# Kernel optimization log

Hardware: AMD Instinct MI355X
Metric: run time of the kernel (lower is better)

The kernel has to match this reference:

```python
import jax, jax.numpy as jnp
import numpy as np

N = 20000      # nodes
E = 320000     # edges (avg degree 16)
IN, HID, OUT, H = 128, 32, 32, 8
NEG_SLOPE = 0.2


def _gat_conv(x, src, dst, W, al, ar, b):
    """One DGL-style GATConv. x: [N, F_in], W: [F_in, H*D], al/ar: [H, D], b: [H*D].
    Returns [N, H, D]."""
    n = x.shape[0]
    Hh, D = al.shape
    feat = (x @ W).reshape(n, Hh, D)                      # [N,H,D]
    el = jnp.sum(feat * al[None], axis=-1)                # [N,H]
    er = jnp.sum(feat * ar[None], axis=-1)                # [N,H]
    e = jax.nn.leaky_relu(el[src] + er[dst], NEG_SLOPE)   # [E,H]
    # edge softmax over incoming edges of each dst node (stable)
    emax = jax.ops.segment_max(e, dst, num_segments=n)    # [N,H]
    ee = jnp.exp(e - emax[dst])                           # [E,H]
    denom = jax.ops.segment_sum(ee, dst, num_segments=n)  # [N,H]
    alpha = ee / denom[dst]                               # [E,H]
    msg = feat[src] * alpha[:, :, None]                   # [E,H,D] gather+weight
    out = jax.ops.segment_sum(msg, dst, num_segments=n)   # [N,H,D] scatter-add
    return out + b.reshape(1, Hh, D)


def setup_inputs() -> dict:
    key = jax.random.key(0)
    ks = jax.random.split(key, 11)
    return {
        "x":   jax.random.normal(ks[0], (N, IN), dtype=jnp.float32),
        "src": jax.random.randint(ks[1], (E,), 0, N, dtype=jnp.int32),
        "dst": jax.random.randint(ks[2], (E,), 0, N, dtype=jnp.int32),
        "W1":  jax.random.normal(ks[3], (IN, H * HID), dtype=jnp.float32) * 0.1,
        "al1": jax.random.normal(ks[4], (H, HID), dtype=jnp.float32) * 0.1,
        "ar1": jax.random.normal(ks[5], (H, HID), dtype=jnp.float32) * 0.1,
        "b1":  jnp.zeros((H * HID,), dtype=jnp.float32),
        "W2":  jax.random.normal(ks[6], (HID, H * OUT), dtype=jnp.float32) * 0.1,
        "al2": jax.random.normal(ks[7], (H, OUT), dtype=jnp.float32) * 0.1,
        "ar2": jax.random.normal(ks[8], (H, OUT), dtype=jnp.float32) * 0.1,
        "b2":  jnp.zeros((H * OUT,), dtype=jnp.float32),
    }


def reference(x, src, dst, W1, al1, ar1, b1, W2, al2, ar2, b2):
    h = _gat_conv(x, src, dst, W1, al1, ar1, b1)          # [N,H,HID]
    h = jnp.mean(jax.nn.relu(h), axis=1)                  # [N,HID]
    h = _gat_conv(h, src, dst, W2, al2, ar2, b2)          # [N,H,OUT]
    return jnp.mean(h, axis=1)                            # [N,OUT]
```

## Files before the change

### kernel.cpp

```cpp
#include <hip/hip_runtime.h>
#include <hip/hip_bf16.h>

#define N_NODES 20000
#define N_EDGES 320000
#define F_IN    128
#define F_HID   32
#define NHEAD   8
#define FDIM    256
#define CAP     96

#define GROUPS  313
#define GPAD    16
#define GCAP    2048
#define EPB     2048
#define P1B     ((N_EDGES + EPB - 1) / EPB)

#define TW2     12

typedef __hip_bfloat16 bf16;
typedef __attribute__((ext_vector_type(8))) short short8;
typedef __attribute__((ext_vector_type(4))) float f32x4;

__device__ __forceinline__ unsigned short f2bf_rne(float f){
  unsigned u = __float_as_uint(f);
  unsigned r = u + 0x7FFFu + ((u >> 16) & 1u);
  return (unsigned short)(r >> 16);
}
__device__ __forceinline__ float bf2f(unsigned short s){
  return __uint_as_float((unsigned)s << 16);
}

__global__ void init_kernel(const float* __restrict__ W1, const float* __restrict__ W2,
                            const float* __restrict__ al2, const float* __restrict__ ar2,
                            int* __restrict__ gcnt,
                            unsigned short* __restrict__ h1, unsigned short* __restrict__ l1,
                            float* __restrict__ q_lt, float* __restrict__ q_rt){
  const int b = blockIdx.x;
  if (b == 0){
    for (int i = threadIdx.x; i < GROUPS*GPAD; i += 256) gcnt[i] = 0;
  } else if (b < 129){
    int i = (b - 1)*256 + threadIdx.x;
    int n = i >> 7, k = i & 127;
    float v = W1[(size_t)k*FDIM + n];
    unsigned short hs = f2bf_rne(v);
    h1[i] = hs;
    l1[i] = f2bf_rne(v - bf2f(hs));
  } else {
    int t = threadIdx.x;
    int k = t >> 3, hh = t & 7;
    float sl = 0.f, sr = 0.f;
    #pragma unroll
    for (int d = 0; d < 32; d++){
      float w = W2[(size_t)k*FDIM + hh*32 + d];
      sl = fmaf(w, al2[hh*32 + d], sl);
      sr = fmaf(w, ar2[hh*32 + d], sr);
    }
    q_lt[t] = sl;
    q_rt[t] = sr;
  }
}

#define GEMMB  (N_NODES / 16)
__global__ __launch_bounds__(256) void gemm_p1_kernel(
    const int* __restrict__ src, const int* __restrict__ dst,
    int* __restrict__ gcnt, unsigned* __restrict__ recs,
    const float* __restrict__ X,
    const unsigned short* __restrict__ Wthi, const unsigned short* __restrict__ Wtlo,
    const float* __restrict__ al, const float* __restrict__ ar,
    unsigned short* __restrict__ feat, float* __restrict__ el, float* __restrict__ er)
{
  const int b = blockIdx.x;
  const int tid = threadIdx.x;

  if (b < P1B){
    __shared__ int hist[GROUPS];
    for (int t = tid; t < GROUPS; t += 256) hist[t] = 0;
    __syncthreads();

    unsigned rec[8]; int bin[8]; bool val[8];
    const int e0 = b * EPB;
    #pragma unroll
    for (int k = 0; k < 8; k++){
      int i = e0 + k*256 + tid;
      val[k] = (i < N_EDGES);
      if (val[k]){
        int s = src[i];
        int d = dst[i];
        bin[k] = d >> 6;
        rec[k] = (unsigned)(((d & 63) << 16) | s);
        atomicAdd(&hist[bin[k]], 1);
      }
    }
    __syncthreads();
    {
      const int rot = (b * 97) % GROUPS;
      for (int tt = tid; tt < GROUPS; tt += 256){
        int t = tt + rot; if (t >= GROUPS) t -= GROUPS;
        int h = hist[t];
        hist[t] = (h > 0) ? atomicAdd(&gcnt[t*GPAD], h) : 0;
      }
    }
    __syncthreads();
    #pragma unroll
    for (int k = 0; k < 8; k++){
      if (val[k]){
        int pos = atomicAdd(&hist[bin[k]], 1);
        if (pos < GCAP) recs[(size_t)bin[k]*GCAP + pos] = rec[k];
      }
    }
    return;
  }

  constexpr int K = F_IN;
  const int wv   = tid >> 6;
  const int lane = tid & 63;
  const int quad = lane >> 4;
  const int l16  = lane & 15;
  const int m0   = (b - P1B) * 16;
  constexpr int NC = K / 32;

  short8 Ah[NC], Al_[NC];
  {
    const float* xrow = X + (size_t)(m0 + l16)*K;
    #pragma unroll
    for (int c = 0; c < NC; c++){
      float4 a0 = *(const float4*)(xrow + c*32 + quad*8);
      float4 a1 = *(const float4*)(xrow + c*32 + quad*8 + 4);
      const float vs[8] = {a0.x,a0.y,a0.z,a0.w,a1.x,a1.y,a1.z,a1.w};
      #pragma unroll
      for (int j = 0; j < 8; j++){
        unsigned short hs = f2bf_rne(vs[j]);
        Ah[c][j]  = (short)hs;
        Al_[c][j] = (short)f2bf_rne(vs[j] - bf2f(hs));
      }
    }
  }

  float elp[8], erp[8];
  #pragma unroll
  for (int j = 0; j < 8; j++){ elp[j] = 0.f; erp[j] = 0.f; }

  #pragma unroll
  for (int t = 0; t < 4; t++){
    const int nc = wv*64 + t*16;
    const size_t brow = (size_t)(nc + l16) * K;
    f32x4 acc = {0.f, 0.f, 0.f, 0.f};
    #pragma unroll
    for (int c = 0; c < NC; c++){
      short8 Bh = *(const short8*)(Wthi + brow + c*32 + quad*8);
      short8 Bl = *(const short8*)(Wtlo + brow + c*32 + quad*8);
      acc = __builtin_amdgcn_mfma_f32_16x16x32_bf16(Ah[c],  Bh, acc, 0, 0, 0);
      acc = __builtin_amdgcn_mfma_f32_16x16x32_bf16(Ah[c],  Bl, acc, 0, 0, 0);
      acc = __builtin_amdgcn_mfma_f32_16x16x32_bf16(Al_[c], Bh, acc, 0, 0, 0);
    }
    const float alv = al[nc + l16];
    const float arv = ar[nc + l16];
    const int hl = t >> 1;
    #pragma unroll
    for (int r = 0; r < 4; r++){
      float v = acc[r];
      feat[(size_t)(m0 + quad*4 + r)*FDIM + nc + l16] = f2bf_rne(v);
      elp[r*2 + hl] = fmaf(v, alv, elp[r*2 + hl]);
      erp[r*2 + hl] = fmaf(v, arv, erp[r*2 + hl]);
    }
  }

  #pragma unroll
  for (int off = 1; off <= 8; off <<= 1){
    #pragma unroll
    for (int j = 0; j < 8; j++){
      elp[j] += __shfl_xor(elp[j], off);
      erp[j] += __shfl_xor(erp[j], off);
    }
  }
  __shared__ float el_lds[16][8], er_lds[16][8];
  if (l16 == 0){
    #pragma unroll
    for (int r = 0; r < 4; r++){
      #pragma unroll
      for (int hl = 0; hl < 2; hl++){
        el_lds[quad*4 + r][wv*2 + hl] = elp[r*2 + hl];
        er_lds[quad*4 + r][wv*2 + hl] = erp[r*2 + hl];
      }
    }
  }
  __syncthreads();
  if (tid < 128){
    int row = tid >> 3, h = tid & 7;
    el[(size_t)(m0 + row)*NHEAD + h] = el_lds[row][h];
    er[(size_t)(m0 + row)*NHEAD + h] = er_lds[row][h];
  }
}

__global__ __launch_bounds__(256) void bucket_build_kernel(
    const unsigned* __restrict__ recs, const int* __restrict__ gcnt,
    int* __restrict__ cnt, int* __restrict__ bucket)
{
  const int g  = blockIdx.x;
  const int n0 = g << 6;
  __shared__ int lcnt[64];
  __shared__ int lbuck[64*CAP];
  if (threadIdx.x < 64) lcnt[threadIdx.x] = 0;
  __syncthreads();

  int m = gcnt[g*GPAD]; if (m > GCAP) m = GCAP;
  for (int r = threadIdx.x; r < m; r += 256){
    unsigned w = recs[(size_t)g*GCAP + r];
    int d = (int)(w >> 16);
    int p = atomicAdd(&lcnt[d], 1);
    if (p < CAP) lbuck[d*CAP + p] = (int)(w & 0xFFFFu);
  }
  __syncthreads();

  int nn = N_NODES - n0; if (nn > 64) nn = 64;
  if (threadIdx.x < nn) cnt[n0 + threadIdx.x] = lcnt[threadIdx.x];
  const int tot4 = (nn * CAP) >> 2;
  int4* gb = (int4*)(bucket + (size_t)n0 * CAP);
  const int4* lb = (const int4*)lbuck;
  for (int i = threadIdx.x; i < tot4; i += 256) gb[i] = lb[i];
}

__global__ __launch_bounds__(64, 6) void edge_agg_l1(
    const bf16* __restrict__ feat, const float* __restrict__ el,
    const float* __restrict__ er, const int* __restrict__ cnt,
    const int* __restrict__ bucket, const float* __restrict__ bias,
    const float* __restrict__ q_lt, const float* __restrict__ q_rt,
    unsigned short* __restrict__ h_out, float* __restrict__ el2,
    float* __restrict__ er2)
{
  const int lane = threadIdx.x;
  const int n    = blockIdx.x;

  __shared__ float t_w[CAP*9];
  __shared__ int   s_w[CAP];
  __shared__ float sum_h[NHEAD];
  __shared__ float v_sh[256];
  __shared__ float h_sh[32];

  int C = cnt[n];
  if (C > CAP) C = CAP;

  const float4* er4 = (const float4*)(er + (size_t)n*NHEAD);
  float4 era = er4[0], erb = er4[1];
  const float erv[8] = {era.x, era.y, era.z, era.w, erb.x, erb.y, erb.z, erb.w};

  for (int idx = lane; idx < C*2; idx += 64){
    const int e = idx >> 1, j = idx & 1;
    const int sidx = bucket[(size_t)n*CAP + e];
    if (j == 0) s_w[e] = sidx;
    float4 a = ((const float4*)(el + (size_t)sidx*NHEAD))[j];
    const float ev[4] = {a.x, a.y, a.z, a.w};
    #pragma unroll
    for (int hh = 0; hh < 4; hh++){
      float v = ev[hh] + erv[j*4 + hh];
      t_w[e*9 + j*4 + hh] = (v > 0.f) ? v : 0.2f*v;
    }
  }
  {
    const int h = lane >> 3, d = lane & 7;
    float lm = -INFINITY;
    for (int e = d; e < C; e += 8) lm = fmaxf(lm, t_w[e*9 + h]);
    #pragma unroll
    for (int off = 4; off >= 1; off >>= 1) lm = fmaxf(lm, __shfl_xor(lm, off));
    float ls = 0.f;
    for (int e = d; e < C; e += 8){
      float ex = __expf(t_w[e*9 + h] - lm);
      t_w[e*9 + h] = ex;
      ls += ex;
    }
    #pragma unroll
    for (int off = 4; off >= 1; off >>= 1) ls += __shfl_xor(ls, off);
    if (d == 0) sum_h[h] = ls;
  }

  const int sub = lane >> 5;
  const int l   = lane & 31;
  const int hB  = l >> 2;
  const int coff = l << 3;
  float acc[8] = {0,0,0,0,0,0,0,0};
  int e = sub;
  float4 fv0, fv1;
  if (e < C)     fv0 = *(const float4*)(feat + (size_t)s_w[e]*FDIM + coff);
  if (e + 2 < C) fv1 = *(const float4*)(feat + (size_t)s_w[e+2]*FDIM + coff);
  while (e < C){
    float4 fnext;
    if (e + 4 < C) fnext = *(const float4*)(feat + (size_t)s_w[e+4]*FDIM + coff);
    const float w = t_w[e*9 + hB];
    const unsigned* u = (const unsigned*)&fv0;
    #pragma unroll
    for (int j = 0; j < 4; j++){
      float flo = __uint_as_float(u[j] << 16);
      float fhi = __uint_as_float(u[j] & 0xFFFF0000u);
      acc[2*j]   = fmaf(w, flo, acc[2*j]);
      acc[2*j+1] = fmaf(w, fhi, acc[2*j+1]);
    }
    fv0 = fv1; fv1 = fnext;
    e += 2;
  }
  #pragma unroll
  for (int j = 0; j < 8; j++) acc[j] += __shfl_xor(acc[j], 32);

  if (lane < 32){
    const float s = sum_h[lane >> 2];
    const float4* b4 = (const float4*)(bias + coff);
    float4 ba = b4[0], bb = b4[1];
    float bv[8] = {ba.x, ba.y, ba.z, ba.w, bb.x, bb.y, bb.z, bb.w};
    float v[8];
    #pragma unroll
    for (int j = 0; j < 8; j++){
      float val = (C > 0) ? (acc[j] / s) : 0.f;
      val += bv[j];
      val = fmaxf(val, 0.f);
      v[j] = val;
    }
    float4* v4 = (float4*)&v_sh[coff];
    v4[0] = make_float4(v[0], v[1], v[2], v[3]);
    v4[1] = make_float4(v[4], v[5], v[6], v[7]);
  }
  if (lane < 32){
    float hsum = 0.f;
    #pragma unroll
    for (int hh = 0; hh < 8; hh++) hsum += v_sh[hh*32 + lane];
    hsum *= 0.125f;
    h_out[(size_t)n*32 + lane] = f2bf_rne(hsum);
    h_sh[lane] = hsum;
  }
  if (lane < 32){
    const int j    = lane & 7;
    const int sel  = (lane >> 3) & 1;
    const int half = lane >> 4;
    const float* qt = sel ? q_rt : q_lt;
    float p = 0.f;
    #pragma unroll
    for (int k = 0; k < 16; k++){
      const int kk = half*16 + k;
      p = fmaf(h_sh[kk], qt[kk*8 + j], p);
    }
    p += __shfl_xor(p, 16);
    if (lane < 8)       el2[(size_t)n*NHEAD + j] = p;
    else if (lane < 16) er2[(size_t)n*NHEAD + j] = p;
  }
}

__global__ __launch_bounds__(256, 6) void edge_agg_l2(
    const unsigned short* __restrict__ h_bf, const float* __restrict__ el2,
    const float* __restrict__ er2, const int* __restrict__ cnt,
    const int* __restrict__ bucket, const float* __restrict__ W2,
    const float* __restrict__ b2, float* __restrict__ outp)
{
  const int tid  = threadIdx.x;
  const int wv   = tid >> 6;
  const int lane = tid & 63;
  const int n    = blockIdx.x*4 + wv;

  __shared__ __align__(16) float t_all[4][CAP*TW2];
  __shared__ int   s_all[4][CAP];
  __shared__ float sum_all[4][NHEAD];
  float* t_w = t_all[wv];
  int*   s_w = s_all[wv];

  int C = cnt[n];
  if (C > CAP) C = CAP;

  const float4* er4 = (const float4*)(er2 + (size_t)n*NHEAD);
  float4 era = er4[0], erb = er4[1];
  const float erv[8] = {era.x, era.y, era.z, era.w, erb.x, erb.y, erb.z, erb.w};

  for (int idx = lane; idx < C*2; idx += 64){
    const int e = idx >> 1, j = idx & 1;
    const int sidx = bucket[(size_t)n*CAP + e];
    if (j == 0) s_w[e] = sidx;
    float4 a = ((const float4*)(el2 + (size_t)sidx*NHEAD))[j];
    const float ev[4] = {a.x, a.y, a.z, a.w};
    #pragma unroll
    for (int hh = 0; hh < 4; hh++){
      float v = ev[hh] + erv[j*4 + hh];
      t_w[e*TW2 + j*4 + hh] = (v > 0.f) ? v : 0.2f*v;
    }
  }
  {
    const int h = lane >> 3, d = lane & 7;
    float lm = -INFINITY;
    for (int e = d; e < C; e += 8) lm = fmaxf(lm, t_w[e*TW2 + h]);
    #pragma unroll
    for (int off = 4; off >= 1; off >>= 1) lm = fmaxf(lm, __shfl_xor(lm, off));
    float ls = 0.f;
    for (int e = d; e < C; e += 8){
      float ex = __expf(t_w[e*TW2 + h] - lm);
      t_w[e*TW2 + h] = ex;
      ls += ex;
    }
    #pragma unroll
    for (int off = 4; off >= 1; off >>= 1) ls += __shfl_xor(ls, off);
    if (d == 0) sum_all[wv][h] = ls;
  }

  const int sub = lane >> 4;
  const int q   = lane & 15;
  float acc[16];
  #pragma unroll
  for (int i = 0; i < 16; i++) acc[i] = 0.f;
  int e = sub;
  unsigned hv;
  if (e < C) hv = *(const unsigned*)(h_bf + (size_t)s_w[e]*32 + q*2);
  while (e < C){
    const int en = e + 4;
    unsigned hnext;
    if (en < C) hnext = *(const unsigned*)(h_bf + (size_t)s_w[en]*32 + q*2);
    f32x4 w0 = *(const f32x4*)&t_w[e*TW2];
    f32x4 w1 = *(const f32x4*)&t_w[e*TW2 + 4];
    const float x0 = __uint_as_float(hv << 16);
    const float x1 = __uint_as_float(hv & 0xFFFF0000u);
    #pragma unroll
    for (int h = 0; h < 4; h++){
      acc[2*h]   = fmaf(w0[h], x0, acc[2*h]);
      acc[2*h+1] = fmaf(w0[h], x1, acc[2*h+1]);
      acc[8+2*h]   = fmaf(w1[h], x0, acc[8+2*h]);
      acc[8+2*h+1] = fmaf(w1[h], x1, acc[8+2*h+1]);
    }
    hv = hnext;
    e = en;
  }
  #pragma unroll
  for (int i = 0; i < 16; i++){
    acc[i] += __shfl_xor(acc[i], 16);
    acc[i] += __shfl_xor(acc[i], 32);
  }
  if (lane < 16){
    #pragma unroll
    for (int h = 0; h < 8; h++){
      const float s = sum_all[wv][h];
      const float inv = (C > 0) ? (1.f / s) : 0.f;
      t_w[h*33 + 2*lane]     = acc[2*h]   * inv;
      t_w[h*33 + 2*lane + 1] = acc[2*h+1] * inv;
    }
  }
  __syncthreads();

  {
    const int c  = tid;
    const int hc = c >> 5;
    float p0=0.f, p1=0.f, p2=0.f, p3=0.f;
    for (int k = 0; k < F_HID; k++){
      float w = W2[(size_t)k*FDIM + c];
      p0 = fmaf(t_all[0][hc*33 + k], w, p0);
      p1 = fmaf(t_all[1][hc*33 + k], w, p1);
      p2 = fmaf(t_all[2][hc*33 + k], w, p2);
      p3 = fmaf(t_all[3][hc*33 + k], w, p3);
    }
    t_all[0][512 + c] = p0;
    t_all[1][512 + c] = p1;
    t_all[2][512 + c] = p2;
    t_all[3][512 + c] = p3;
  }
  __syncthreads();
  if (tid < 128){
    const int nn = tid >> 5, d = tid & 31;
    float s = 0.f, bm = 0.f;
    #pragma unroll
    for (int hh = 0; hh < 8; hh++){
      s  += t_all[nn][512 + hh*32 + d];
      bm += b2[hh*32 + d];
    }
    outp[(size_t)(blockIdx.x*4 + nn)*32 + d] = (s + bm) * 0.125f;
  }
}

extern "C" void kernel_launch(void* const* d_in, const int* in_sizes, int n_in,
                              void* d_out, int out_size, void* d_ws, size_t ws_size,
                              hipStream_t stream)
{
  const float* x   = (const float*)d_in[0];
  const int*   src = (const int*)  d_in[1];
  const int*   dst = (const int*)  d_in[2];
  const float* W1  = (const float*)d_in[3];
  const float* al1 = (const float*)d_in[4];
  const float* ar1 = (const float*)d_in[5];
  const float* b1  = (const float*)d_in[6];
  const float* W2  = (const float*)d_in[7];
  const float* al2 = (const float*)d_in[8];
  const float* ar2 = (const float*)d_in[9];
  const float* b2  = (const float*)d_in[10];
  (void)in_sizes; (void)n_in; (void)out_size; (void)ws_size;

  size_t o = 0;
  char* base = (char*)d_ws;
  auto take = [&](size_t bytes) -> char* {
    char* p = base + o;
    o += (bytes + 255) & ~(size_t)255;
    return p;
  };
  unsigned short* feat  = (unsigned short*)take((size_t)N_NODES*FDIM*2);
  float* el1    = (float*)take((size_t)N_NODES*NHEAD*4);
  float* er1    = (float*)take((size_t)N_NODES*NHEAD*4);
  float* el2    = (float*)take((size_t)N_NODES*NHEAD*4);
  float* er2    = (float*)take((size_t)N_NODES*NHEAD*4);
  int*   cnt    = (int*)  take((size_t)N_NODES*4);
  int*   bucket = (int*)  take((size_t)N_NODES*CAP*4);
  unsigned short* hbf  = (unsigned short*)take((size_t)N_NODES*F_HID*2);
  unsigned short* W1th = (unsigned short*)take((size_t)FDIM*F_IN*2);
  unsigned short* W1tl = (unsigned short*)take((size_t)FDIM*F_IN*2);
  float* q_lt   = (float*)take((size_t)F_HID*NHEAD*4);
  float* q_rt   = (float*)take((size_t)F_HID*NHEAD*4);
  int*   gcnt   = (int*)  take((size_t)GROUPS*GPAD*4);
  unsigned* recs = (unsigned*)take((size_t)GROUPS*GCAP*4);

  init_kernel<<<130, 256, 0, stream>>>(
      W1, W2, al2, ar2, gcnt, W1th, W1tl, q_lt, q_rt);

  gemm_p1_kernel<<<P1B + GEMMB, 256, 0, stream>>>(
      src, dst, gcnt, recs, x, W1th, W1tl, al1, ar1, feat, el1, er1);

  bucket_build_kernel<<<GROUPS, 256, 0, stream>>>(recs, gcnt, cnt, bucket);

  edge_agg_l1<<<N_NODES, 64, 0, stream>>>(
      (const bf16*)feat, el1, er1, cnt, bucket, b1, q_lt, q_rt, hbf, el2, er2);

  edge_agg_l2<<<N_NODES/4, 256, 0, stream>>>(
      hbf, el2, er2, cnt, bucket, W2, b2, (float*)d_out);
}
```

Baseline: 170.3 us.

## Locally sort edge records by bin before global scatter; copy only filled bucket slots

The edge-binning pass now doubles the edges per block, counts a histogram, prefix-sums it in shared memory, and places records into a shared sorted array. Each bin's records are then written to global memory contiguously, which should coalesce scatter writes and halve the number of global atomics per bin. The bucket build kernel now copies only the occupied slots of each node's bucket rather than the full CAP region, cutting global write traffic. In exchange, the binning pass reads src/dst twice, uses more shared memory, and runs fewer blocks, which may lower parallelism.

```diff
diff --git a/kernel.cpp b/kernel.cpp
--- a/kernel.cpp
+++ b/kernel.cpp
@@ -12,7 +12,7 @@
 #define GROUPS  313
 #define GPAD    16
 #define GCAP    2048
-#define EPB     2048
+#define EPB     4096
 #define P1B     ((N_EDGES + EPB - 1) / EPB)
 
 #define TW2     12
@@ -74,39 +74,61 @@
 
   if (b < P1B){
     __shared__ int hist[GROUPS];
+    __shared__ int prefix[GROUPS];
+    __shared__ int chunktot[16];
+    __shared__ unsigned sorted[EPB];
+
     for (int t = tid; t < GROUPS; t += 256) hist[t] = 0;
     __syncthreads();
 
-    unsigned rec[8]; int bin[8]; bool val[8];
     const int e0 = b * EPB;
-    #pragma unroll
-    for (int k = 0; k < 8; k++){
+    const int nval = min(EPB, N_EDGES - e0);
+    for (int k = 0; k < EPB/256; k++){
       int i = e0 + k*256 + tid;
-      val[k] = (i < N_EDGES);
-      if (val[k]){
-        int s = src[i];
-        int d = dst[i];
-        bin[k] = d >> 6;
-        rec[k] = (unsigned)(((d & 63) << 16) | s);
-        atomicAdd(&hist[bin[k]], 1);
+      if (i < N_EDGES) atomicAdd(&hist[dst[i] >> 6], 1);
+    }
+    __syncthreads();
+    if (tid < 16){
+      int base = tid*20, run = 0;
+      for (int c = 0; c < 20; c++){
+        int t = base + c;
+        if (t < GROUPS){ prefix[t] = run; run += hist[t]; }
       }
-    }
+      chunktot[tid] = run;
+    }
+    __syncthreads();
+    if (tid == 0){
+      int run = 0;
+      #pragma unroll
+      for (int c = 0; c < 16; c++){ int t = chunktot[c]; chunktot[c] = run; run += t; }
+    }
+    __syncthreads();
+    for (int t = tid; t < GROUPS; t += 256) prefix[t] += chunktot[t/20];
     __syncthreads();
     {
       const int rot = (b * 97) % GROUPS;
       for (int tt = tid; tt < GROUPS; tt += 256){
         int t = tt + rot; if (t >= GROUPS) t -= GROUPS;
         int h = hist[t];
-        hist[t] = (h > 0) ? atomicAdd(&gcnt[t*GPAD], h) : 0;
+        int g = (h > 0) ? atomicAdd(&gcnt[t*GPAD], h) : 0;
+        hist[t] = g - prefix[t];
       }
     }
     __syncthreads();
-    #pragma unroll
-    for (int k = 0; k < 8; k++){
-      if (val[k]){
-        int pos = atomicAdd(&hist[bin[k]], 1);
-        if (pos < GCAP) recs[(size_t)bin[k]*GCAP + pos] = rec[k];
+    for (int k = 0; k < EPB/256; k++){
+      int i = e0 + k*256 + tid;
+      if (i < N_EDGES){
+        int s = src[i], d = dst[i];
+        int slot = atomicAdd(&prefix[d >> 6], 1);
+        sorted[slot] = (unsigned)((d << 16) | s);
       }
+    }
+    __syncthreads();
+    for (int j = tid; j < nval; j += 256){
+      unsigned rec = sorted[j];
+      int bin = (int)(rec >> 22);
+      int off = hist[bin] + j;
+      if (off < GCAP) recs[(size_t)bin*GCAP + off] = rec;
     }
     return;
   }
@@ -206,18 +228,23 @@
   int m = gcnt[g*GPAD]; if (m > GCAP) m = GCAP;
   for (int r = threadIdx.x; r < m; r += 256){
     unsigned w = recs[(size_t)g*GCAP + r];
-    int d = (int)(w >> 16);
+    int d = (int)((w >> 16) & 63);
     int p = atomicAdd(&lcnt[d], 1);
     if (p < CAP) lbuck[d*CAP + p] = (int)(w & 0xFFFFu);
   }
   __syncthreads();
 
-  int nn = N_NODES - n0; if (nn > 64) nn = 64;
-  if (threadIdx.x < nn) cnt[n0 + threadIdx.x] = lcnt[threadIdx.x];
-  const int tot4 = (nn * CAP) >> 2;
-  int4* gb = (int4*)(bucket + (size_t)n0 * CAP);
-  const int4* lb = (const int4*)lbuck;
-  for (int i = threadIdx.x; i < tot4; i += 256) gb[i] = lb[i];
+  const int nn = min(64, N_NODES - n0);
+  const int d = threadIdx.x >> 2, j = threadIdx.x & 3;
+  if (d < nn){
+    int c = lcnt[d];
+    if (j == 0) cnt[n0 + d] = c;
+    if (c > CAP) c = CAP;
+    const int n4 = (c + 3) >> 2;
+    int4* gb = (int4*)(bucket + (size_t)(n0 + d)*CAP);
+    const int4* lb = (const int4*)(lbuck + d*CAP);
+    for (int i = j; i < n4; i += 4) gb[i] = lb[i];
+  }
 }
 
 __global__ __launch_bounds__(64, 6) void edge_agg_l1(
```

New measurement: 171.9 us. No clear change (+0.9%).

## Widen per-lane feature loads in layer-1 aggregation and copy only filled bucket entries

Applied to the files above, without the earlier changes.

The layer-1 edge aggregation now has each lane handle 16 bf16 features (two float4 loads per edge) with four edge sub-groups and a deeper prefetch, reducing across lanes with two shuffle steps. Per-edge attention logits are computed one edge per lane and written as aligned float4 stores into a 12-float stride buffer. The bucket build kernel now copies only the occupied slots of each node's bucket instead of the full CAP region, cutting global write traffic. The trade-off is higher register pressure from the 16 accumulators and changed LDS bank behaviour from the wider padded stride.

```diff
diff --git a/kernel.cpp b/kernel.cpp
--- a/kernel.cpp
+++ b/kernel.cpp
@@ -15,6 +15,7 @@
 #define EPB     2048
 #define P1B     ((N_EDGES + EPB - 1) / EPB)
 
+#define TW1     12
 #define TW2     12
 
 typedef __hip_bfloat16 bf16;
@@ -206,18 +207,23 @@
   int m = gcnt[g*GPAD]; if (m > GCAP) m = GCAP;
   for (int r = threadIdx.x; r < m; r += 256){
     unsigned w = recs[(size_t)g*GCAP + r];
-    int d = (int)(w >> 16);
+    int d = (int)((w >> 16) & 63);
     int p = atomicAdd(&lcnt[d], 1);
     if (p < CAP) lbuck[d*CAP + p] = (int)(w & 0xFFFFu);
   }
   __syncthreads();
 
-  int nn = N_NODES - n0; if (nn > 64) nn = 64;
-  if (threadIdx.x < nn) cnt[n0 + threadIdx.x] = lcnt[threadIdx.x];
-  const int tot4 = (nn * CAP) >> 2;
-  int4* gb = (int4*)(bucket + (size_t)n0 * CAP);
-  const int4* lb = (const int4*)lbuck;
-  for (int i = threadIdx.x; i < tot4; i += 256) gb[i] = lb[i];
+  const int nn = min(64, N_NODES - n0);
+  const int d = threadIdx.x >> 2, j = threadIdx.x & 3;
+  if (d < nn){
+    int c = lcnt[d];
+    if (j == 0) cnt[n0 + d] = c;
+    if (c > CAP) c = CAP;
+    const int n4 = (c + 3) >> 2;
+    int4* gb = (int4*)(bucket + (size_t)(n0 + d)*CAP);
+    const int4* lb = (const int4*)(lbuck + d*CAP);
+    for (int i = j; i < n4; i += 4) gb[i] = lb[i];
+  }
 }
 
 __global__ __launch_bounds__(64, 6) void edge_agg_l1(
@@ -231,7 +237,7 @@
   const int lane = threadIdx.x;
   const int n    = blockIdx.x;
 
-  __shared__ float t_w[CAP*9];
+  __shared__ __align__(16) float t_w[CAP*TW1];
   __shared__ int   s_w[CAP];
   __shared__ float sum_h[NHEAD];
   __shared__ float v_sh[256];
@@ -244,28 +250,29 @@
   float4 era = er4[0], erb = er4[1];
   const float erv[8] = {era.x, era.y, era.z, era.w, erb.x, erb.y, erb.z, erb.w};
 
-  for (int idx = lane; idx < C*2; idx += 64){
-    const int e = idx >> 1, j = idx & 1;
+  for (int e = lane; e < C; e += 64){
     const int sidx = bucket[(size_t)n*CAP + e];
-    if (j == 0) s_w[e] = sidx;
-    float4 a = ((const float4*)(el + (size_t)sidx*NHEAD))[j];
-    const float ev[4] = {a.x, a.y, a.z, a.w};
-    #pragma unroll
-    for (int hh = 0; hh < 4; hh++){
-      float v = ev[hh] + erv[j*4 + hh];
-      t_w[e*9 + j*4 + hh] = (v > 0.f) ? v : 0.2f*v;
-    }
+    s_w[e] = sidx;
+    const float4* e4 = (const float4*)(el + (size_t)sidx*NHEAD);
+    float4 a = e4[0], bq = e4[1];
+    float v[8] = {a.x + erv[0], a.y + erv[1], a.z + erv[2], a.w + erv[3],
+                  bq.x + erv[4], bq.y + erv[5], bq.z + erv[6], bq.w + erv[7]};
+    #pragma unroll
+    for (int hh = 0; hh < 8; hh++) v[hh] = (v[hh] > 0.f) ? v[hh] : 0.2f*v[hh];
+    float4* tw4 = (float4*)&t_w[e*TW1];
+    tw4[0] = make_float4(v[0], v[1], v[2], v[3]);
+    tw4[1] = make_float4(v[4], v[5], v[6], v[7]);
   }
   {
     const int h = lane >> 3, d = lane & 7;
     float lm = -INFINITY;
-    for (int e = d; e < C; e += 8) lm = fmaxf(lm, t_w[e*9 + h]);
+    for (int e = d; e < C; e += 8) lm = fmaxf(lm, t_w[e*TW1 + h]);
     #pragma unroll
     for (int off = 4; off >= 1; off >>= 1) lm = fmaxf(lm, __shfl_xor(lm, off));
     float ls = 0.f;
     for (int e = d; e < C; e += 8){
-      float ex = __expf(t_w[e*9 + h] - lm);
-      t_w[e*9 + h] = ex;
+      float ex = __expf(t_w[e*TW1 + h] - lm);
+      t_w[e*TW1 + h] = ex;
       ls += ex;
     }
     #pragma unroll
@@ -273,49 +280,63 @@
     if (d == 0) sum_h[h] = ls;
   }
 
-  const int sub = lane >> 5;
-  const int l   = lane & 31;
-  const int hB  = l >> 2;
-  const int coff = l << 3;
-  float acc[8] = {0,0,0,0,0,0,0,0};
+  const int sub  = lane >> 4;
+  const int q    = lane & 15;
+  const int hB   = q >> 1;
+  const int coff = q << 4;
+  float acc[16];
+  #pragma unroll
+  for (int i = 0; i < 16; i++) acc[i] = 0.f;
   int e = sub;
-  float4 fv0, fv1;
-  if (e < C)     fv0 = *(const float4*)(feat + (size_t)s_w[e]*FDIM + coff);
-  if (e + 2 < C) fv1 = *(const float4*)(feat + (size_t)s_w[e+2]*FDIM + coff);
+  float4 fa0, fb0, fa1, fb1;
+  if (e < C){
+    const float4* r = (const float4*)(feat + (size_t)s_w[e]*FDIM + coff);
+    fa0 = r[0]; fb0 = r[1];
+  }
+  if (e + 4 < C){
+    const float4* r = (const float4*)(feat + (size_t)s_w[e+4]*FDIM + coff);
+    fa1 = r[0]; fb1 = r[1];
+  }
   while (e < C){
-    float4 fnext;
-    if (e + 4 < C) fnext = *(const float4*)(feat + (size_t)s_w[e+4]*FDIM + coff);
-    const float w = t_w[e*9 + hB];
-    const unsigned* u = (const unsigned*)&fv0;
+    float4 na, nb;
+    if (e + 8 < C){
+      const float4* r = (const float4*)(feat + (size_t)s_w[e+8]*FDIM + coff);
+      na = r[0]; nb = r[1];
+    }
+    const float w = t_w[e*TW1 + hB];
+    const unsigned* ua = (const unsigned*)&fa0;
+    const unsigned* ub = (const unsigned*)&fb0;
     #pragma unroll
     for (int j = 0; j < 4; j++){
-      float flo = __uint_as_float(u[j] << 16);
-      float fhi = __uint_as_float(u[j] & 0xFFFF0000u);
-      acc[2*j]   = fmaf(w, flo, acc[2*j]);
-      acc[2*j+1] = fmaf(w, fhi, acc[2*j+1]);
-    }
-    fv0 = fv1; fv1 = fnext;
-    e += 2;
-  }
-  #pragma unroll
-  for (int j = 0; j < 8; j++) acc[j] += __shfl_xor(acc[j], 32);
-
-  if (lane < 32){
-    const float s = sum_h[lane >> 2];
+      acc[2*j]      = fmaf(w, __uint_as_float(ua[j] << 16),        acc[2*j]);
+      acc[2*j+1]    = fmaf(w, __uint_as_float(ua[j] & 0xFFFF0000u), acc[2*j+1]);
+      acc[8+2*j]    = fmaf(w, __uint_as_float(ub[j] << 16),        acc[8+2*j]);
+      acc[8+2*j+1]  = fmaf(w, __uint_as_float(ub[j] & 0xFFFF0000u), acc[8+2*j+1]);
+    }
+    fa0 = fa1; fb0 = fb1; fa1 = na; fb1 = nb;
+    e += 4;
+  }
+  #pragma unroll
+  for (int i = 0; i < 16; i++){
+    acc[i] += __shfl_xor(acc[i], 16);
+    acc[i] += __shfl_xor(acc[i], 32);
+  }
+
+  if (lane < 16){
+    const float s = sum_h[hB];
+    const float inv = (C > 0) ? (1.f / s) : 0.f;
     const float4* b4 = (const float4*)(bias + coff);
-    float4 ba = b4[0], bb = b4[1];
-    float bv[8] = {ba.x, ba.y, ba.z, ba.w, bb.x, bb.y, bb.z, bb.w};
-    float v[8];
-    #pragma unroll
-    for (int j = 0; j < 8; j++){
-      float val = (C > 0) ? (acc[j] / s) : 0.f;
-      val += bv[j];
-      val = fmaxf(val, 0.f);
-      v[j] = val;
-    }
     float4* v4 = (float4*)&v_sh[coff];
-    v4[0] = make_float4(v[0], v[1], v[2], v[3]);
-    v4[1] = make_float4(v[4], v[5], v[6], v[7]);
+    #pragma unroll
+    for (int g = 0; g < 4; g++){
+      float4 bv = b4[g];
+      float4 ov;
+      ov.x = fmaxf(acc[4*g+0]*inv + bv.x, 0.f);
+      ov.y = fmaxf(acc[4*g+1]*inv + bv.y, 0.f);
+      ov.z = fmaxf(acc[4*g+2]*inv + bv.z, 0.f);
+      ov.w = fmaxf(acc[4*g+3]*inv + bv.w, 0.f);
+      v4[g] = ov;
+    }
   }
   if (lane < 32){
     float hsum = 0.f;
```

Measured after the change: 168.8 us. No clear change (-0.9%).
